# Optimization experiments

Measured on AMD Instinct MI355X. Metric: run time of the kernel, lower is better.

Reference implementation:

```python
import jax, jax.numpy as jnp
import numpy as np

B = 512      # batch of scenes
K = 16       # entities (slots) per scene
H = 500      # h == HIDDEN_SIZE (required by fc2 input width 2*HIDDEN_SIZE)
A = 64       # action_size
EPS = 1e-5


def layernorm(x, g, b):
    mu = jnp.mean(x, axis=-1, keepdims=True)
    var = jnp.var(x, axis=-1, keepdims=True)
    return (x - mu) * jax.lax.rsqrt(var + EPS) * g + b


def setup_inputs() -> dict:
    key = jax.random.key(0)
    ks = jax.random.split(key, 40)
    def W(i, shape, scale=0.02):
        return (jax.random.normal(ks[i], shape, dtype=jnp.float32) * scale)
    inp = {
        "state": jax.random.normal(ks[0], (B * K, H), dtype=jnp.float32),
        "actions": jax.random.normal(ks[1], (B, A), dtype=jnp.float32),
        # action path
        "ac_fc1_w": W(2, (A, H)), "ac_fc1_b": jnp.zeros((H,), jnp.float32),
        "ac_ln1_g": jnp.ones((H,), jnp.float32), "ac_ln1_b": jnp.zeros((H,), jnp.float32),
        "ac_fc2_w": W(3, (2 * H, H)), "ac_fc2_b": jnp.zeros((H,), jnp.float32),
        "ac_lnf2_w": W(4, (H, H)), "ac_lnf2_b": jnp.zeros((H,), jnp.float32),  # ac_ln_f2 is a Linear in the source
        "ac_fc3_w": W(5, (2 * H, 1)), "ac_fc3_b": jnp.zeros((1,), jnp.float32),
        # main path
        "fc1_w": W(6, (H, H)), "fc1_b": jnp.zeros((H,), jnp.float32),
        "ln1_g": jnp.ones((H,), jnp.float32), "ln1_b": jnp.zeros((H,), jnp.float32),
        "fc2_w": W(7, (2 * H, H)), "fc2_b": jnp.zeros((H,), jnp.float32),
        "ln2_g": jnp.ones((H,), jnp.float32), "ln2_b": jnp.zeros((H,), jnp.float32),
        "fc3_w": W(8, (H, H)), "fc3_b": jnp.zeros((H,), jnp.float32),
        "ln3_g": jnp.ones((H,), jnp.float32), "ln3_b": jnp.zeros((H,), jnp.float32),
        "fc4_w": W(9, (H, 100)), "fc4_b": jnp.zeros((100,), jnp.float32),
        "ln4_g": jnp.ones((100,), jnp.float32), "ln4_b": jnp.zeros((100,), jnp.float32),
        "fc5_w": W(10, (100, 1)), "fc5_b": jnp.zeros((1,), jnp.float32),
        "fc6_w": W(11, (2 * H, H)), "fc6_b": jnp.zeros((H,), jnp.float32),
        "ln6_g": jnp.ones((H,), jnp.float32), "ln6_b": jnp.zeros((H,), jnp.float32),
    }
    return inp


def reference(state, actions,
              ac_fc1_w, ac_fc1_b, ac_ln1_g, ac_ln1_b,
              ac_fc2_w, ac_fc2_b, ac_lnf2_w, ac_lnf2_b, ac_fc3_w, ac_fc3_b,
              fc1_w, fc1_b, ln1_g, ln1_b,
              fc2_w, fc2_b, ln2_g, ln2_b,
              fc3_w, fc3_b, ln3_g, ln3_b,
              fc4_w, fc4_b, ln4_g, ln4_b,
              fc5_w, fc5_b,
              fc6_w, fc6_b, ln6_g, ln6_b):
    b, k, h, nc = B, K, H, K - 1

    # ---- action_forward (has_action=True) ----
    a = layernorm(actions @ ac_fc1_w + ac_fc1_b, ac_ln1_g, ac_ln1_b)      # [b, h]
    a = jnp.broadcast_to(a[:, None, :], (b, k, h)).reshape(b * k, h)       # repeat over k
    concat_a = jnp.concatenate([state, a], axis=1)                          # [b*k, 2h]
    attention_a = jax.nn.sigmoid(concat_a @ ac_fc3_w + ac_fc3_b)           # [b*k, 1]
    effect = (concat_a @ ac_fc2_w + ac_fc2_b) @ ac_lnf2_w + ac_lnf2_b      # ac_ln_f2 is Linear
    state = effect * attention_a                                            # [b*k, h]

    # ---- per-entity encoder ----
    s1 = jax.nn.relu(layernorm(state @ fc1_w + fc1_b, ln1_g, ln1_b))       # [b*k, h]
    s1r = s1.reshape(b, k, h)

    # ---- all-pairs context gather: for each i, all j != i ----
    idx = np.array([[j for j in range(k) if j != i] for i in range(k)])    # [k, k-1] static
    cs = s1r[:, idx, :]                                                     # [b, k, k-1, h]
    fs = jnp.broadcast_to(s1r[:, :, None, :], (b, k, nc, h))               # [b, k, k-1, h]
    pair = jnp.concatenate([fs, cs], axis=-1).reshape(b * k * nc, 2 * h)   # [b*k*(k-1), 2h]

    # ---- edge MLP ----
    core = jax.nn.relu(layernorm(pair @ fc2_w + fc2_b, ln2_g, ln2_b))      # [b*k*nc, h]
    context = jax.nn.relu(layernorm(core @ fc3_w + fc3_b, ln3_g, ln3_b))
    context = context.reshape(b * k, nc, h)

    # ---- attention-weighted sum aggregation ----
    att = jnp.tanh(layernorm(core @ fc4_w + fc4_b, ln4_g, ln4_b))          # [b*k*nc, 100]
    att = jax.nn.sigmoid(att @ fc5_w + fc5_b).reshape(b * k, nc, 1)
    effect_sum = jnp.sum(context * att, axis=1)                             # [b*k, h]

    # ---- update ----
    total = jnp.concatenate([s1, effect_sum], axis=1)                       # [b*k, 2h]
    h_new = layernorm(total @ fc6_w + fc6_b, ln6_g, ln6_b)                  # [b*k, h]
    return h_new
```

## Files before the change

kernel.cpp:

```cpp
#include <hip/hip_runtime.h>
#include <math.h>


#define EPSF 1e-5f
typedef unsigned short u16;
typedef unsigned int u32;

typedef __bf16 bf16x8 __attribute__((ext_vector_type(8)));
typedef float f32x4 __attribute__((ext_vector_type(4)));
typedef u16 u16x8 __attribute__((ext_vector_type(8)));

__device__ __forceinline__ float bf2f(u16 u) {
  return __builtin_bit_cast(float, (u32)u << 16);
}
__device__ __forceinline__ u16 f2bf(float f) {
  u32 u = __builtin_bit_cast(u32, f);
  return (u16)((u + 0x7FFFu + ((u >> 16) & 1u)) >> 16);
}

#define GLOAD16(g, l) __builtin_amdgcn_global_load_lds( \
    (__attribute__((address_space(1))) u32*)(g), \
    (__attribute__((address_space(3))) u32*)(l), 16, 0, 0)

template <typename TOUT>
__global__ __launch_bounds__(256) void gemm_mfma(
    const u16* __restrict__ A, const u16* __restrict__ A2,
    const u16* __restrict__ Bt,
    const float* __restrict__ bias, const float* __restrict__ rowscale,
    TOUT* __restrict__ C, int M, int Npad, int K, int lda, int khalf)
{
  __shared__ __align__(16) u16 As[2][128 * 64];
  __shared__ __align__(16) u16 Bs[2][64 * 64];
  const int tid = threadIdx.x;
  const int lane = tid & 63, wid = tid >> 6;

  const int ncols = gridDim.x;
  const int nwg = ncols * gridDim.y;
  const int bid = blockIdx.y * ncols + blockIdx.x;
  const int swz = (bid & 7) * (nwg >> 3) + (bid >> 3);
  const size_t row0 = (size_t)(swz / ncols) * 128;
  const size_t col0 = (size_t)(swz % ncols) * 64;

  f32x4 acc[2][4] = {};

  const int s_sub = tid >> 3;
  const int s_chunk = (tid & 7) ^ (s_sub & 7);
  const size_t aoff = (row0 + s_sub) * (size_t)lda + s_chunk * 8;
  const u16* gA = A + aoff;
  const u16* gA2 = A2 ? (A2 + aoff - khalf) : nullptr;
  const u16* gB = Bt + (col0 + s_sub) * (size_t)K + s_chunk * 8;

  const int fr = lane & 15, fq = lane >> 4;
  const int cx0 = fq ^ (fr & 7);
  const int cx1 = (4 + fq) ^ (fr & 7);

  const int nkt = K >> 6;
  int cur = 0;

  {
#pragma unroll
    for (int h = 0; h < 4; ++h)
      GLOAD16(gA + (size_t)h * 32 * lda, &As[0][(h * 256 + tid) * 8]);
#pragma unroll
    for (int h = 0; h < 2; ++h)
      GLOAD16(gB + (size_t)h * 32 * K, &Bs[0][(h * 256 + tid) * 8]);
  }

  for (int kt = 0; kt < nkt; ++kt) {
    if (kt + 1 < nkt) {
      const int kk = (kt + 1) * 64;
      const u16* a = (A2 && kk >= khalf) ? (gA2 + kk) : (gA + kk);
      const u16* b = gB + kk;
#pragma unroll
      for (int h = 0; h < 4; ++h)
        GLOAD16(a + (size_t)h * 32 * lda, &As[cur ^ 1][(h * 256 + tid) * 8]);
#pragma unroll
      for (int h = 0; h < 2; ++h)
        GLOAD16(b + (size_t)h * 32 * K, &Bs[cur ^ 1][(h * 256 + tid) * 8]);
      asm volatile("s_waitcnt vmcnt(6)" ::: "memory");
    } else {
      asm volatile("s_waitcnt vmcnt(0)" ::: "memory");
    }
    __builtin_amdgcn_sched_barrier(0);
    __builtin_amdgcn_s_barrier();
    __builtin_amdgcn_sched_barrier(0);

    const u16* as = As[cur];
    const u16* bs = Bs[cur];
#pragma unroll
    for (int ks = 0; ks < 2; ++ks) {
      const int cx = ks ? cx1 : cx0;
      bf16x8 af[2], bf[4];
#pragma unroll
      for (int m = 0; m < 2; ++m) {
        int row = wid * 32 + m * 16 + fr;
        af[m] = *reinterpret_cast<const bf16x8*>(as + (row * 8 + cx) * 8);
      }
#pragma unroll
      for (int n = 0; n < 4; ++n) {
        int row = n * 16 + fr;
        bf[n] = *reinterpret_cast<const bf16x8*>(bs + (row * 8 + cx) * 8);
      }
#pragma unroll
      for (int m = 0; m < 2; ++m)
#pragma unroll
        for (int n = 0; n < 4; ++n)
          acc[m][n] = __builtin_amdgcn_mfma_f32_16x16x32_bf16(af[m], bf[n], acc[m][n], 0, 0, 0);
    }
    asm volatile("s_waitcnt lgkmcnt(0)" ::: "memory");
    __builtin_amdgcn_sched_barrier(0);
    __builtin_amdgcn_s_barrier();
    __builtin_amdgcn_sched_barrier(0);
    cur ^= 1;
  }

  const int cl = lane & 15, rg = lane >> 4;
#pragma unroll
  for (int m = 0; m < 2; ++m) {
#pragma unroll
    for (int n = 0; n < 4; ++n) {
      size_t col = col0 + n * 16 + cl;
      float bv = bias[col];
#pragma unroll
      for (int r = 0; r < 4; ++r) {
        size_t row = row0 + wid * 32 + m * 16 + rg * 4 + r;
        float v = acc[m][n][r] + bv;
        if (rowscale) v *= rowscale[row];
        if constexpr (sizeof(TOUT) == 2) C[row * Npad + col] = f2bf(v);
        else                             C[row * Npad + col] = v;
      }
    }
  }
}

template <typename TOUT>
__global__ __launch_bounds__(256) void gemm_sq(
    const u16* __restrict__ A, const u16* __restrict__ Bt,
    const float* __restrict__ bias,
    TOUT* __restrict__ C, int M, int Npad, int K, int lda)
{
  __shared__ __align__(16) u16 As[128 * 64];
  __shared__ __align__(16) u16 Bs[128 * 64];
  const int tid = threadIdx.x;
  const int lane = tid & 63, wid = tid >> 6;
  const int ar0 = (wid >> 1) * 64;
  const int bc0 = (wid & 1) * 64;

  const int ncols = gridDim.x;
  const int nwg = ncols * gridDim.y;
  const int bid = blockIdx.y * ncols + blockIdx.x;
  const int swz = (bid & 7) * (nwg >> 3) + (bid >> 3);
  const size_t row0 = (size_t)(swz / ncols) * 128;
  const size_t col0 = (size_t)(swz % ncols) * 128;

  f32x4 acc[4][4] = {};

  const int s_sub = tid >> 3;
  const int s_chunk = (tid & 7) ^ (s_sub & 7);
  const u16* gA = A + (row0 + s_sub) * (size_t)lda + s_chunk * 8;
  const u16* gB = Bt + (col0 + s_sub) * (size_t)K + s_chunk * 8;

  const int fr = lane & 15, fq = lane >> 4;
  const int cx0 = fq ^ (fr & 7);
  const int cx1 = (4 + fq) ^ (fr & 7);

  for (int kk = 0; kk < K; kk += 64) {
#pragma unroll
    for (int h = 0; h < 4; ++h) {
      GLOAD16(gA + kk + (size_t)h * 32 * lda, &As[(h * 256 + tid) * 8]);
      GLOAD16(gB + kk + (size_t)h * 32 * K,  &Bs[(h * 256 + tid) * 8]);
    }
    __syncthreads();
#pragma unroll
    for (int ks = 0; ks < 2; ++ks) {
      const int cx = ks ? cx1 : cx0;
      bf16x8 af[4], bf[4];
#pragma unroll
      for (int m = 0; m < 4; ++m)
        af[m] = *reinterpret_cast<const bf16x8*>(As + ((ar0 + m * 16 + fr) * 8 + cx) * 8);
#pragma unroll
      for (int n = 0; n < 4; ++n)
        bf[n] = *reinterpret_cast<const bf16x8*>(Bs + ((bc0 + n * 16 + fr) * 8 + cx) * 8);
#pragma unroll
      for (int m = 0; m < 4; ++m)
#pragma unroll
        for (int n = 0; n < 4; ++n)
          acc[m][n] = __builtin_amdgcn_mfma_f32_16x16x32_bf16(af[m], bf[n], acc[m][n], 0, 0, 0);
    }
    __syncthreads();
  }

  const int cl = lane & 15, rg = lane >> 4;
#pragma unroll
  for (int m = 0; m < 4; ++m) {
#pragma unroll
    for (int n = 0; n < 4; ++n) {
      size_t col = col0 + bc0 + n * 16 + cl;
      float bv = bias[col];
#pragma unroll
      for (int r = 0; r < 4; ++r) {
        size_t row = row0 + ar0 + m * 16 + rg * 4 + r;
        float v = acc[m][n][r] + bv;
        if constexpr (sizeof(TOUT) == 2) C[row * Npad + col] = f2bf(v);
        else                             C[row * Npad + col] = v;
      }
    }
  }
}

__global__ __launch_bounds__(256) void gemm128(
    const float* __restrict__ A, const float* __restrict__ B,
    const float* __restrict__ bias, float* __restrict__ C, int M, int N, int K)
{
  __shared__ float As[16][132];
  __shared__ float Bs[16][128];
  const int tid = threadIdx.x;
  const int tx = tid & 15, ty = tid >> 4;
  const int row0 = blockIdx.y * 128, col0 = blockIdx.x * 128;
  float acc[8][8];
#pragma unroll
  for (int i = 0; i < 8; ++i)
#pragma unroll
    for (int j = 0; j < 8; ++j) acc[i][j] = 0.f;

  const int nkt = (K + 15) >> 4;
  for (int kt = 0; kt < nkt; ++kt) {
    const int k0 = kt << 4;
#pragma unroll
    for (int h = 0; h < 2; ++h) {
      int i = tid + h * 256;
      int m = i >> 2, kk = (i & 3) << 2;
      int gm = row0 + m, gk = k0 + kk;
      float4 v = make_float4(0.f, 0.f, 0.f, 0.f);
      if (gm < M && gk < K) v = *reinterpret_cast<const float4*>(A + (size_t)gm * K + gk);
      As[kk + 0][m] = v.x; As[kk + 1][m] = v.y; As[kk + 2][m] = v.z; As[kk + 3][m] = v.w;
    }
#pragma unroll
    for (int h = 0; h < 2; ++h) {
      int i = tid + h * 256;
      int kk = i >> 5, n = (i & 31) << 2;
      int gk = k0 + kk, gn = col0 + n;
      float4 v = make_float4(0.f, 0.f, 0.f, 0.f);
      if (gk < K && gn < N) v = *reinterpret_cast<const float4*>(B + (size_t)gk * N + gn);
      *reinterpret_cast<float4*>(&Bs[kk][n]) = v;
    }
    __syncthreads();
#pragma unroll
    for (int kk = 0; kk < 16; ++kk) {
      float4 a0 = *reinterpret_cast<const float4*>(&As[kk][ty * 4]);
      float4 a1 = *reinterpret_cast<const float4*>(&As[kk][ty * 4 + 64]);
      float4 b0 = *reinterpret_cast<const float4*>(&Bs[kk][tx * 4]);
      float4 b1 = *reinterpret_cast<const float4*>(&Bs[kk][tx * 4 + 64]);
      float av[8] = {a0.x, a0.y, a0.z, a0.w, a1.x, a1.y, a1.z, a1.w};
      float bv[8] = {b0.x, b0.y, b0.z, b0.w, b1.x, b1.y, b1.z, b1.w};
#pragma unroll
      for (int i = 0; i < 8; ++i)
#pragma unroll
        for (int j = 0; j < 8; ++j) acc[i][j] += av[i] * bv[j];
    }
    __syncthreads();
  }
#pragma unroll
  for (int i = 0; i < 8; ++i) {
    int gm = row0 + ty * 4 + ((i >> 2) << 6) + (i & 3);
    if (gm >= M) continue;
#pragma unroll
    for (int j = 0; j < 8; ++j) {
      int gn = col0 + tx * 4 + ((j >> 2) << 6) + (j & 3);
      if (gn < N) C[(size_t)gm * N + gn] = acc[i][j] + bias[gn];
    }
  }
}

template <int ACT, typename TIN, typename TOUT>
__global__ __launch_bounds__(256) void ln_wave4(
    const TIN* __restrict__ X, TOUT* __restrict__ Y,
    const float* __restrict__ g, const float* __restrict__ b,
    int ldx, int ldy)
{
  int w = threadIdx.x >> 6, lane = threadIdx.x & 63;
  int id0 = (blockIdx.x * 4 + w) * 4;
  int k0 = lane * 8;
  float xv[4][8], s[4], s2[4];
#pragma unroll
  for (int r = 0; r < 4; ++r) {
    s[r] = 0.f; s2[r] = 0.f;
    if constexpr (sizeof(TIN) == 2) {
      u16x8 u = *reinterpret_cast<const u16x8*>((const u16*)X + (size_t)(id0 + r) * ldx + k0);
#pragma unroll
      for (int e = 0; e < 8; ++e) xv[r][e] = bf2f(u[e]);
    } else {
      const float* x = (const float*)X + (size_t)(id0 + r) * ldx;
      if (k0 + 8 <= 500) {
        float4 a = *reinterpret_cast<const float4*>(x + k0);
        float4 c = *reinterpret_cast<const float4*>(x + k0 + 4);
        xv[r][0] = a.x; xv[r][1] = a.y; xv[r][2] = a.z; xv[r][3] = a.w;
        xv[r][4] = c.x; xv[r][5] = c.y; xv[r][6] = c.z; xv[r][7] = c.w;
      } else {
#pragma unroll
        for (int e = 0; e < 8; ++e) xv[r][e] = (k0 + e < 500) ? x[k0 + e] : 0.f;
      }
    }
#pragma unroll
    for (int e = 0; e < 8; ++e) { s[r] += xv[r][e]; s2[r] += xv[r][e] * xv[r][e]; }
  }
#pragma unroll
  for (int m = 32; m; m >>= 1)
#pragma unroll
    for (int r = 0; r < 4; ++r) {
      s[r] += __shfl_xor(s[r], m);
      s2[r] += __shfl_xor(s2[r], m);
    }
  float gv[8], bv[8];
#pragma unroll
  for (int e = 0; e < 8; ++e) {
    int k = k0 + e;
    gv[e] = (k < 500) ? g[k] : 0.f;
    bv[e] = (k < 500) ? b[k] : 0.f;
  }
#pragma unroll
  for (int r = 0; r < 4; ++r) {
    float mu = s[r] / 500.f;
    float rstd = rsqrtf(s2[r] / 500.f - mu * mu + EPSF);
    float ov[8];
#pragma unroll
    for (int e = 0; e < 8; ++e) {
      float v = (k0 + e < 500) ? ((xv[r][e] - mu) * rstd * gv[e] + bv[e]) : 0.f;
      if (ACT == 1) v = fmaxf(v, 0.f);
      ov[e] = v;
    }
    if constexpr (sizeof(TOUT) == 2) {
      u16x8 o;
#pragma unroll
      for (int e = 0; e < 8; ++e) o[e] = f2bf(ov[e]);
      *reinterpret_cast<u16x8*>((u16*)Y + (size_t)(id0 + r) * ldy + k0) = o;
    } else {
      float* y = (float*)Y + (size_t)(id0 + r) * ldy;
      if (k0 + 4 <= 500)
        *reinterpret_cast<float4*>(y + k0) = make_float4(ov[0], ov[1], ov[2], ov[3]);
      if (k0 + 8 <= 500)
        *reinterpret_cast<float4*>(y + k0 + 4) = make_float4(ov[4], ov[5], ov[6], ov[7]);
    }
  }
}

__global__ __launch_bounds__(256) void build_concat(
    const float* __restrict__ state, const u16* __restrict__ a, u16* __restrict__ cat)
{
  int r = blockIdx.x, t = threadIdx.x;
  int b = r >> 4;
  u16* c = cat + (size_t)r * 1024;
  if (t < 125) {
    float4 v = *reinterpret_cast<const float4*>(state + (size_t)r * 500 + t * 4);
    ushort4 o; o.x = f2bf(v.x); o.y = f2bf(v.y); o.z = f2bf(v.z); o.w = f2bf(v.w);
    *reinterpret_cast<ushort4*>(c + t * 4) = o;
    *reinterpret_cast<ushort4*>(c + 500 + t * 4) =
        *reinterpret_cast<const ushort4*>(a + (size_t)b * 512 + t * 4);
  }
  if (t < 24) c[1000 + t] = 0;
}

__global__ __launch_bounds__(256) void dot_sig4(
    const u16* __restrict__ cat, const float* __restrict__ w3,
    const float* __restrict__ b3, float* __restrict__ atta)
{
  int w = threadIdx.x >> 6, lane = threadIdx.x & 63;
  int r0 = (blockIdx.x * 4 + w) * 4;
  int k0 = lane * 16;
  float wv[16];
#pragma unroll
  for (int e = 0; e < 16; ++e) wv[e] = (k0 + e < 1000) ? w3[k0 + e] : 0.f;
  float s[4];
#pragma unroll
  for (int r = 0; r < 4; ++r) {
    const u16* x = cat + (size_t)(r0 + r) * 1024 + k0;
    u16x8 u0 = *reinterpret_cast<const u16x8*>(x);
    u16x8 u1 = *reinterpret_cast<const u16x8*>(x + 8);
    float acc = 0.f;
#pragma unroll
    for (int e = 0; e < 8; ++e) acc += bf2f(u0[e]) * wv[e];
#pragma unroll
    for (int e = 0; e < 8; ++e) acc += bf2f(u1[e]) * wv[8 + e];
    s[r] = acc;
  }
#pragma unroll
  for (int m = 32; m; m >>= 1)
#pragma unroll
    for (int r = 0; r < 4; ++r) s[r] += __shfl_xor(s[r], m);
  if (lane == 0) {
#pragma unroll
    for (int r = 0; r < 4; ++r)
      atta[r0 + r] = 1.f / (1.f + expf(-(s[r] + b3[0])));
  }
}

__global__ __launch_bounds__(256) void core_build3(
    const u16* __restrict__ PQ, u16* __restrict__ core,
    const float* __restrict__ g2, const float* __restrict__ b2, int c0)
{
  int w = threadIdx.x >> 6, lane = threadIdx.x & 63;
  int id0 = (blockIdx.x * 4 + w) * 4;
  int k0 = lane * 8;
  u16x8 up[4], uq[4];
#pragma unroll
  for (int r = 0; r < 4; ++r) {
    int id = id0 + r;
    int pp = id / 15, j = id - pp * 15;
    int gp = c0 + pp, i = gp & 15;
    int col = j + (j >= i);
    int r2 = (gp & ~15) | col;
    up[r] = *reinterpret_cast<const u16x8*>(PQ + (size_t)gp * 1024 + k0);
    uq[r] = *reinterpret_cast<const u16x8*>(PQ + (size_t)r2 * 1024 + 512 + k0);
  }
  float xv[4][8], s[4], s2[4];
#pragma unroll
  for (int r = 0; r < 4; ++r) {
    s[r] = 0.f; s2[r] = 0.f;
#pragma unroll
    for (int e = 0; e < 8; ++e) {
      float v = bf2f(up[r][e]) + bf2f(uq[r][e]);
      xv[r][e] = v; s[r] += v; s2[r] += v * v;
    }
  }
#pragma unroll
  for (int m = 32; m; m >>= 1)
#pragma unroll
    for (int r = 0; r < 4; ++r) {
      s[r] += __shfl_xor(s[r], m);
      s2[r] += __shfl_xor(s2[r], m);
    }
  float gv[8], bv[8];
#pragma unroll
  for (int e = 0; e < 8; ++e) {
    int k = k0 + e;
    gv[e] = (k < 500) ? g2[k] : 0.f;
    bv[e] = (k < 500) ? b2[k] : 0.f;
  }
#pragma unroll
  for (int r = 0; r < 4; ++r) {
    float mu = s[r] / 500.f;
    float rstd = rsqrtf(s2[r] / 500.f - mu * mu + EPSF);
    u16x8 o;
#pragma unroll
    for (int e = 0; e < 8; ++e)
      o[e] = (k0 + e < 500) ? f2bf(fmaxf((xv[r][e] - mu) * rstd * gv[e] + bv[e], 0.f)) : (u16)0;
    *reinterpret_cast<u16x8*>(core + (size_t)(id0 + r) * 512 + k0) = o;
  }
}

__global__ __launch_bounds__(256) void chunk_post3(
    const u16* __restrict__ V,
    const float* __restrict__ g3, const float* __restrict__ b3,
    const float* __restrict__ g4, const float* __restrict__ b4,
    const float* __restrict__ w5, const float* __restrict__ b5,
    u16* __restrict__ esum16, int c0)
{
  __shared__ u16 rows[15][512];
  __shared__ float st[15][4];
  int pp = blockIdx.x, t = threadIdx.x;
  int lane = t & 63, w = t >> 6;
  int k0 = lane * 8;
  int kk = lane * 2;

  u16x8 u[4]; ushort2 ua[4];
#pragma unroll
  for (int r = 0; r < 4; ++r) {
    int j = w * 4 + r;
    if (j < 15) {
      const u16* vr = V + (size_t)(pp * 15 + j) * 640;
      u[r] = *reinterpret_cast<const u16x8*>(vr + k0);
      ua[r] = *reinterpret_cast<const ushort2*>(vr + 512 + kk);
    }
  }
  float s[4], s2[4], sa[4], sa2[4], y0[4], y1[4];
#pragma unroll
  for (int r = 0; r < 4; ++r) {
    s[r] = s2[r] = sa[r] = sa2[r] = 0.f; y0[r] = y1[r] = 0.f;
    int j = w * 4 + r;
    if (j < 15) {
#pragma unroll
      for (int e = 0; e < 8; ++e) { float v = bf2f(u[r][e]); s[r] += v; s2[r] += v * v; }
      y0[r] = bf2f(ua[r].x); y1[r] = bf2f(ua[r].y);
      sa[r] = y0[r] + y1[r]; sa2[r] = y0[r] * y0[r] + y1[r] * y1[r];
      *reinterpret_cast<u16x8*>(&rows[j][k0]) = u[r];
    }
  }
#pragma unroll
  for (int m = 32; m; m >>= 1)
#pragma unroll
    for (int r = 0; r < 4; ++r) {
      s[r]   += __shfl_xor(s[r], m);
      s2[r]  += __shfl_xor(s2[r], m);
      sa[r]  += __shfl_xor(sa[r], m);
      sa2[r] += __shfl_xor(sa2[r], m);
    }
  float dv[4];
#pragma unroll
  for (int r = 0; r < 4; ++r) {
    float mu4 = sa[r] / 100.f;
    float rstd4 = rsqrtf(sa2[r] / 100.f - mu4 * mu4 + EPSF);
    float d = 0.f;
    if (kk < 100)     d += tanhf((y0[r] - mu4) * rstd4 * g4[kk] + b4[kk]) * w5[kk];
    if (kk + 1 < 100) d += tanhf((y1[r] - mu4) * rstd4 * g4[kk + 1] + b4[kk + 1]) * w5[kk + 1];
    dv[r] = d;
  }
#pragma unroll
  for (int m = 32; m; m >>= 1)
#pragma unroll
    for (int r = 0; r < 4; ++r) dv[r] += __shfl_xor(dv[r], m);
  if (lane == 0) {
#pragma unroll
    for (int r = 0; r < 4; ++r) {
      int j = w * 4 + r;
      if (j < 15) {
        float mu = s[r] / 500.f;
        st[j][0] = mu;
        st[j][1] = rsqrtf(s2[r] / 500.f - mu * mu + EPSF);
        st[j][2] = 1.f / (1.f + expf(-(dv[r] + b5[0])));
      }
    }
  }
  __syncthreads();

  u16* o = esum16 + (size_t)(c0 + pp) * 512;
  for (int n = t; n < 500; n += 256) {
    float gg = g3[n], bb = b3[n], acc = 0.f;
#pragma unroll
    for (int j = 0; j < 15; ++j) {
      float v = bf2f(rows[j][n]);
      acc += fmaxf((v - st[j][0]) * st[j][1] * gg + bb, 0.f) * st[j][2];
    }
    o[n] = f2bf(acc);
  }
  if (t < 12) o[500 + t] = 0;
}

struct TJob {
  const float* src; u16* dst;
  int K, N, srcLd, ldDst, nOff, kOff, tileBase, tilesX;
};
struct TJobs { TJob j[9]; int total; };

__global__ void pack_weights(TJobs jobs)
{
  __shared__ float tl[32][33];
  int bid = blockIdx.x;
  int ji = 0;
#pragma unroll
  for (int q = 1; q < 9; ++q) if (bid >= jobs.j[q].tileBase) ji = q;
  const TJob& J = jobs.j[ji];
  int t = bid - J.tileBase;
  int bx = t % J.tilesX, by = t / J.tilesX;
  int tx = threadIdx.x, ty = threadIdx.y;
  int k0 = by * 32, n0 = bx * 32;
#pragma unroll
  for (int r = 0; r < 4; ++r) {
    int row = k0 + ty + r * 8;
    if (row < J.K && n0 + tx < J.N) tl[ty + r * 8][tx] = J.src[(size_t)row * J.srcLd + n0 + tx];
  }
  __syncthreads();
#pragma unroll
  for (int r = 0; r < 4; ++r) {
    int n = n0 + ty + r * 8, k = k0 + tx;
    if (n < J.N && k < J.K)
      J.dst[(size_t)(n + J.nOff) * J.ldDst + J.kOff + k] = f2bf(tl[tx][ty + r * 8]);
  }
}

__global__ void pack_biases(
    const float* ac2, const float* lnf2, const float* f1, const float* f2,
    const float* f3, const float* f4, const float* f6,
    float* b_ac2p, float* b_lnf2p, float* b_f1p, float* b2p, float* b34p, float* b_f6p)
{
  int t = threadIdx.x;
  switch (blockIdx.x) {
    case 0: if (t < 512) b_ac2p[t]  = (t < 500) ? ac2[t]  : 0.f; break;
    case 1: if (t < 512) b_lnf2p[t] = (t < 500) ? lnf2[t] : 0.f; break;
    case 2: if (t < 512) b_f1p[t]   = (t < 500) ? f1[t]   : 0.f; break;
    case 3: b2p[t] = (t < 500) ? f2[t] : 0.f; break;
    case 4: if (t < 640) b34p[t] = (t < 500) ? f3[t] : ((t >= 512 && t < 612) ? f4[t - 512] : 0.f); break;
    case 5: if (t < 512) b_f6p[t]   = (t < 500) ? f6[t]   : 0.f; break;
  }
}

extern "C" void kernel_launch(void* const* d_in, const int* in_sizes, int n_in,
                              void* d_out, int out_size, void* d_ws, size_t ws_size,
                              hipStream_t stream)
{
  const float* state    = (const float*)d_in[0];
  const float* actions  = (const float*)d_in[1];
  const float* ac_fc1_w = (const float*)d_in[2];
  const float* ac_fc1_b = (const float*)d_in[3];
  const float* ac_ln1_g = (const float*)d_in[4];
  const float* ac_ln1_b = (const float*)d_in[5];
  const float* ac_fc2_w = (const float*)d_in[6];
  const float* ac_fc2_b = (const float*)d_in[7];
  const float* ac_lnf2_w= (const float*)d_in[8];
  const float* ac_lnf2_b= (const float*)d_in[9];
  const float* ac_fc3_w = (const float*)d_in[10];
  const float* ac_fc3_b = (const float*)d_in[11];
  const float* fc1_w = (const float*)d_in[12];
  const float* fc1_b = (const float*)d_in[13];
  const float* ln1_g = (const float*)d_in[14];
  const float* ln1_b = (const float*)d_in[15];
  const float* fc2_w = (const float*)d_in[16];
  const float* fc2_b = (const float*)d_in[17];
  const float* ln2_g = (const float*)d_in[18];
  const float* ln2_b = (const float*)d_in[19];
  const float* fc3_w = (const float*)d_in[20];
  const float* fc3_b = (const float*)d_in[21];
  const float* ln3_g = (const float*)d_in[22];
  const float* ln3_b = (const float*)d_in[23];
  const float* fc4_w = (const float*)d_in[24];
  const float* fc4_b = (const float*)d_in[25];
  const float* ln4_g = (const float*)d_in[26];
  const float* ln4_b = (const float*)d_in[27];
  const float* fc5_w = (const float*)d_in[28];
  const float* fc5_b = (const float*)d_in[29];
  const float* fc6_w = (const float*)d_in[30];
  const float* fc6_b = (const float*)d_in[31];
  const float* ln6_g = (const float*)d_in[32];
  const float* ln6_b = (const float*)d_in[33];
  float* out = (float*)d_out;

  char* p = (char*)d_ws;
  auto carve = [&](size_t bytes) { char* r = p; p += (bytes + 255) & ~(size_t)255; return r; };
  u16*   cat    = (u16*)  carve(8192ull * 1024 * 2);
  u16*   t1     = (u16*)  carve(8192ull * 512 * 2);
  u16*   s2     = (u16*)  carve(8192ull * 512 * 2);
  u16*   s1     = (u16*)  carve(8192ull * 512 * 2);
  u16*   core   = (u16*)  carve(61440ull * 512 * 2);
  u16*   v      = (u16*)  carve(61440ull * 640 * 2);
  u16*   PQ     = (u16*)  carve(8192ull * 1024 * 2);
  u16*   esum16 = (u16*)  carve(8192ull * 512 * 2);
  u16*   a_buf  = (u16*)  carve(512ull * 512 * 2);
  float* tmp_a  = (float*)carve(512ull * 500 * 4);
  float* att_a  = (float*)carve(8192ull * 4);
  char*  wT0    =         carve(0);
  u16*   ac_fc2T  = (u16*)carve(512ull * 1024 * 2);
  u16*   ac_lnf2T = (u16*)carve(512ull * 512 * 2);
  u16*   fc1T     = (u16*)carve(512ull * 512 * 2);
  u16*   B2T      = (u16*)carve(1024ull * 512 * 2);
  u16*   B34T     = (u16*)carve(640ull * 512 * 2);
  u16*   fc6T     = (u16*)carve(512ull * 1024 * 2);
  size_t wTbytes  = (size_t)((char*)carve(0) - wT0);
  float* b_ac2p  = (float*)carve(512 * 4);
  float* b_lnf2p = (float*)carve(512 * 4);
  float* b_f1p   = (float*)carve(512 * 4);
  float* b2p     = (float*)carve(1024 * 4);
  float* b34p    = (float*)carve(640 * 4);
  float* b_f6p   = (float*)carve(512 * 4);

  dim3 blk(256);
  dim3 tblk(32, 8);

  hipMemsetAsync(wT0, 0, wTbytes, stream);
  TJobs jobs;
  int base = 0;
  auto addjob = [&](int idx, const float* src, u16* dst, int K, int N, int srcLd,
                    int ldDst, int nOff, int kOff) {
    int tx = (N + 31) / 32, ty = (K + 31) / 32;
    jobs.j[idx] = {src, dst, K, N, srcLd, ldDst, nOff, kOff, base, tx};
    base += tx * ty;
  };
  addjob(0, ac_fc2_w,         ac_fc2T,  1000, 500, 500, 1024, 0, 0);
  addjob(1, ac_lnf2_w,        ac_lnf2T,  500, 500, 500,  512, 0, 0);
  addjob(2, fc1_w,            fc1T,      500, 500, 500,  512, 0, 0);
  addjob(3, fc2_w,            B2T,       500, 500, 500,  512, 0, 0);
  addjob(4, fc2_w + 250000,   B2T,       500, 500, 500,  512, 512, 0);
  addjob(5, fc3_w,            B34T,      500, 500, 500,  512, 0, 0);
  addjob(6, fc4_w,            B34T,      500, 100, 100,  512, 512, 0);
  addjob(7, fc6_w,            fc6T,      500, 500, 500, 1024, 0, 0);
  addjob(8, fc6_w + 250000,   fc6T,      500, 500, 500, 1024, 0, 512);
  jobs.total = base;
  pack_weights<<<base, tblk, 0, stream>>>(jobs);
  pack_biases<<<6, 1024, 0, stream>>>(ac_fc2_b, ac_lnf2_b, fc1_b, fc2_b, fc3_b, fc4_b, fc6_b,
                                      b_ac2p, b_lnf2p, b_f1p, b2p, b34p, b_f6p);

  gemm128<<<dim3(4, 4), blk, 0, stream>>>(actions, ac_fc1_w, ac_fc1_b, tmp_a, 512, 500, 64);
  ln_wave4<0, float, u16><<<32, blk, 0, stream>>>(tmp_a, a_buf, ac_ln1_g, ac_ln1_b, 500, 512);
  build_concat<<<8192, blk, 0, stream>>>(state, a_buf, cat);

  gemm_mfma<u16><<<dim3(8, 64), blk, 0, stream>>>(cat, nullptr, ac_fc2T, b_ac2p, nullptr,
                                                  t1, 8192, 512, 1024, 1024, 0);
  dot_sig4<<<512, blk, 0, stream>>>(cat, ac_fc3_w, ac_fc3_b, att_a);
  gemm_mfma<u16><<<dim3(8, 64), blk, 0, stream>>>(t1, nullptr, ac_lnf2T, b_lnf2p, att_a,
                                                  s2, 8192, 512, 512, 512, 0);
  gemm_mfma<u16><<<dim3(8, 64), blk, 0, stream>>>(s2, nullptr, fc1T, b_f1p, nullptr,
                                                  t1, 8192, 512, 512, 512, 0);
  ln_wave4<1, u16, u16><<<512, blk, 0, stream>>>(t1, s1, ln1_g, ln1_b, 512, 512);
  gemm_mfma<u16><<<dim3(16, 64), blk, 0, stream>>>(s1, nullptr, B2T, b2p, nullptr,
                                                   PQ, 8192, 1024, 512, 512, 0);

  for (int c = 0; c < 2; ++c) {
    int c0 = c * 4096;
    core_build3<<<3840, blk, 0, stream>>>(PQ, core, ln2_g, ln2_b, c0);
    gemm_sq<u16><<<dim3(5, 480), blk, 0, stream>>>(core, B34T, b34p,
                                                   v, 61440, 640, 512, 512);
    chunk_post3<<<4096, blk, 0, stream>>>(v, ln3_g, ln3_b, ln4_g, ln4_b, fc5_w, fc5_b,
                                          esum16, c0);
  }

  gemm_mfma<u16><<<dim3(8, 64), blk, 0, stream>>>(s1, esum16, fc6T, b_f6p, nullptr,
                                                  t1, 8192, 512, 1024, 512, 512);
  ln_wave4<0, u16, float><<<512, blk, 0, stream>>>(t1, out, ln6_g, ln6_b, 512, 500);
}
```

Before: 427.5 us.

## Fold three chained linear layers into one precomputed weight product

The three consecutive GEMMs (ac_fc2, ac_lnf2 with row scaling by the attention scalar, then fc1) have no nonlinearity between them. They are collapsed into one 8192x1024x512 GEMM against a precomputed product W_ac2·W_lnf2·W_fc1. The folded bias is applied as rowscale*(b_ac2·W_lnf2·W_fc1 + b_lnf2·W_fc1) + b_fc1. Small per-call GEMMs and matvecs build the fused weight and bias, removing two large GEMMs and an intermediate buffer. The cost is extra bf16 rounding in the precomputed product and a few extra small launches.

```diff
diff --git a/kernel.cpp b/kernel.cpp
--- a/kernel.cpp
+++ b/kernel.cpp
@@ -22,12 +22,13 @@
     (__attribute__((address_space(1))) u32*)(g), \
     (__attribute__((address_space(3))) u32*)(l), 16, 0, 0)
 
-template <typename TOUT>
+template <typename TOUT, bool TRANSC = false>
 __global__ __launch_bounds__(256) void gemm_mfma(
     const u16* __restrict__ A, const u16* __restrict__ A2,
     const u16* __restrict__ Bt,
     const float* __restrict__ bias, const float* __restrict__ rowscale,
-    TOUT* __restrict__ C, int M, int Npad, int K, int lda, int khalf)
+    const float* __restrict__ bias2,
+    TOUT* __restrict__ C, int M, int Npad, int K, int lda, int khalf, int ldc)
 {
   __shared__ __align__(16) u16 As[2][128 * 64];
   __shared__ __align__(16) u16 Bs[2][64 * 64];
@@ -121,13 +122,24 @@
     for (int n = 0; n < 4; ++n) {
       size_t col = col0 + n * 16 + cl;
       float bv = bias[col];
-#pragma unroll
-      for (int r = 0; r < 4; ++r) {
-        size_t row = row0 + wid * 32 + m * 16 + rg * 4 + r;
-        float v = acc[m][n][r] + bv;
-        if (rowscale) v *= rowscale[row];
-        if constexpr (sizeof(TOUT) == 2) C[row * Npad + col] = f2bf(v);
-        else                             C[row * Npad + col] = v;
+      if constexpr (TRANSC) {
+        size_t row0m = row0 + wid * 32 + m * 16 + rg * 4;
+        ushort4 o;
+        o.x = f2bf(acc[m][n][0] + bv);
+        o.y = f2bf(acc[m][n][1] + bv);
+        o.z = f2bf(acc[m][n][2] + bv);
+        o.w = f2bf(acc[m][n][3] + bv);
+        *reinterpret_cast<ushort4*>((u16*)C + col * (size_t)ldc + row0m) = o;
+      } else {
+#pragma unroll
+        for (int r = 0; r < 4; ++r) {
+          size_t row = row0 + wid * 32 + m * 16 + rg * 4 + r;
+          float v = acc[m][n][r] + bv;
+          if (rowscale) v *= rowscale[row];
+          if (bias2) v += bias2[col];
+          if constexpr (sizeof(TOUT) == 2) C[row * (size_t)ldc + col] = f2bf(v);
+          else                             C[row * (size_t)ldc + col] = v;
+        }
       }
     }
   }
@@ -394,6 +406,20 @@
   }
 }
 
+__global__ __launch_bounds__(256) void matvec_col(
+    const float* __restrict__ x, const float* __restrict__ W,
+    const float* __restrict__ add, float* __restrict__ y, int J, int N, int ld)
+{
+  int n = blockIdx.x * 256 + threadIdx.x;
+  if (n >= 512) return;
+  float acc = 0.f;
+  if (n < N) {
+    for (int j = 0; j < J; ++j) acc += x[j] * W[(size_t)j * ld + n];
+    if (add) acc += add[n];
+  }
+  y[n] = acc;
+}
+
 __global__ __launch_bounds__(256) void core_build3(
     const u16* __restrict__ PQ, u16* __restrict__ core,
     const float* __restrict__ g2, const float* __restrict__ b2, int c0)
@@ -537,7 +563,7 @@
 
 struct TJob {
   const float* src; u16* dst;
-  int K, N, srcLd, ldDst, nOff, kOff, tileBase, tilesX;
+  int K, N, srcLd, ldDst, nOff, kOff, tileBase, tilesX, trans;
 };
 struct TJobs { TJob j[9]; int total; };
 
@@ -553,33 +579,41 @@
   int bx = t % J.tilesX, by = t / J.tilesX;
   int tx = threadIdx.x, ty = threadIdx.y;
   int k0 = by * 32, n0 = bx * 32;
-#pragma unroll
-  for (int r = 0; r < 4; ++r) {
-    int row = k0 + ty + r * 8;
-    if (row < J.K && n0 + tx < J.N) tl[ty + r * 8][tx] = J.src[(size_t)row * J.srcLd + n0 + tx];
-  }
-  __syncthreads();
-#pragma unroll
-  for (int r = 0; r < 4; ++r) {
-    int n = n0 + ty + r * 8, k = k0 + tx;
-    if (n < J.N && k < J.K)
-      J.dst[(size_t)(n + J.nOff) * J.ldDst + J.kOff + k] = f2bf(tl[tx][ty + r * 8]);
+  if (J.trans) {
+#pragma unroll
+    for (int r = 0; r < 4; ++r) {
+      int row = k0 + ty + r * 8;
+      if (row < J.K && n0 + tx < J.N) tl[ty + r * 8][tx] = J.src[(size_t)row * J.srcLd + n0 + tx];
+    }
+    __syncthreads();
+#pragma unroll
+    for (int r = 0; r < 4; ++r) {
+      int n = n0 + ty + r * 8, k = k0 + tx;
+      if (n < J.N && k < J.K)
+        J.dst[(size_t)(n + J.nOff) * J.ldDst + J.kOff + k] = f2bf(tl[tx][ty + r * 8]);
+    }
+  } else {
+#pragma unroll
+    for (int r = 0; r < 4; ++r) {
+      int row = k0 + ty + r * 8, n = n0 + tx;
+      if (row < J.K && n < J.N)
+        J.dst[(size_t)(row + J.kOff) * J.ldDst + J.nOff + n] =
+            f2bf(J.src[(size_t)row * J.srcLd + n]);
+    }
   }
 }
 
 __global__ void pack_biases(
-    const float* ac2, const float* lnf2, const float* f1, const float* f2,
-    const float* f3, const float* f4, const float* f6,
-    float* b_ac2p, float* b_lnf2p, float* b_f1p, float* b2p, float* b34p, float* b_f6p)
+    const float* f1, const float* f2, const float* f3, const float* f4,
+    const float* f6,
+    float* b_f1p, float* b2p, float* b34p, float* b_f6p)
 {
   int t = threadIdx.x;
   switch (blockIdx.x) {
-    case 0: if (t < 512) b_ac2p[t]  = (t < 500) ? ac2[t]  : 0.f; break;
-    case 1: if (t < 512) b_lnf2p[t] = (t < 500) ? lnf2[t] : 0.f; break;
-    case 2: if (t < 512) b_f1p[t]   = (t < 500) ? f1[t]   : 0.f; break;
-    case 3: b2p[t] = (t < 500) ? f2[t] : 0.f; break;
-    case 4: if (t < 640) b34p[t] = (t < 500) ? f3[t] : ((t >= 512 && t < 612) ? f4[t - 512] : 0.f); break;
-    case 5: if (t < 512) b_f6p[t]   = (t < 500) ? f6[t]   : 0.f; break;
+    case 0: if (t < 512) b_f1p[t] = (t < 500) ? f1[t] : 0.f; break;
+    case 1: b2p[t] = (t < 500) ? f2[t] : 0.f; break;
+    case 2: if (t < 640) b34p[t] = (t < 500) ? f3[t] : ((t >= 512 && t < 612) ? f4[t - 512] : 0.f); break;
+    case 3: if (t < 512) b_f6p[t] = (t < 500) ? f6[t] : 0.f; break;
   }
 }
 
@@ -627,7 +661,6 @@
   auto carve = [&](size_t bytes) { char* r = p; p += (bytes + 255) & ~(size_t)255; return r; };
   u16*   cat    = (u16*)  carve(8192ull * 1024 * 2);
   u16*   t1     = (u16*)  carve(8192ull * 512 * 2);
-  u16*   s2     = (u16*)  carve(8192ull * 512 * 2);
   u16*   s1     = (u16*)  carve(8192ull * 512 * 2);
   u16*   core   = (u16*)  carve(61440ull * 512 * 2);
   u16*   v      = (u16*)  carve(61440ull * 640 * 2);
@@ -637,19 +670,22 @@
   float* tmp_a  = (float*)carve(512ull * 500 * 4);
   float* att_a  = (float*)carve(8192ull * 4);
   char*  wT0    =         carve(0);
-  u16*   ac_fc2T  = (u16*)carve(512ull * 1024 * 2);
+  u16*   ac_fc2P  = (u16*)carve(1024ull * 512 * 2);
   u16*   ac_lnf2T = (u16*)carve(512ull * 512 * 2);
   u16*   fc1T     = (u16*)carve(512ull * 512 * 2);
   u16*   B2T      = (u16*)carve(1024ull * 512 * 2);
   u16*   B34T     = (u16*)carve(640ull * 512 * 2);
   u16*   fc6T     = (u16*)carve(512ull * 1024 * 2);
+  u16*   W12      = (u16*)carve(1024ull * 512 * 2);
+  u16*   W3T      = (u16*)carve(512ull * 1024 * 2);
+  float* z512     = (float*)carve(512 * 4);
   size_t wTbytes  = (size_t)((char*)carve(0) - wT0);
-  float* b_ac2p  = (float*)carve(512 * 4);
-  float* b_lnf2p = (float*)carve(512 * 4);
   float* b_f1p   = (float*)carve(512 * 4);
   float* b2p     = (float*)carve(1024 * 4);
   float* b34p    = (float*)carve(640 * 4);
   float* b_f6p   = (float*)carve(512 * 4);
+  float* t512    = (float*)carve(512 * 4);
+  float* c3      = (float*)carve(512 * 4);
 
   dim3 blk(256);
   dim3 tblk(32, 8);
@@ -658,39 +694,44 @@
   TJobs jobs;
   int base = 0;
   auto addjob = [&](int idx, const float* src, u16* dst, int K, int N, int srcLd,
-                    int ldDst, int nOff, int kOff) {
+                    int ldDst, int nOff, int kOff, int trans) {
     int tx = (N + 31) / 32, ty = (K + 31) / 32;
-    jobs.j[idx] = {src, dst, K, N, srcLd, ldDst, nOff, kOff, base, tx};
+    jobs.j[idx] = {src, dst, K, N, srcLd, ldDst, nOff, kOff, base, tx, trans};
     base += tx * ty;
   };
-  addjob(0, ac_fc2_w,         ac_fc2T,  1000, 500, 500, 1024, 0, 0);
-  addjob(1, ac_lnf2_w,        ac_lnf2T,  500, 500, 500,  512, 0, 0);
-  addjob(2, fc1_w,            fc1T,      500, 500, 500,  512, 0, 0);
-  addjob(3, fc2_w,            B2T,       500, 500, 500,  512, 0, 0);
-  addjob(4, fc2_w + 250000,   B2T,       500, 500, 500,  512, 512, 0);
-  addjob(5, fc3_w,            B34T,      500, 500, 500,  512, 0, 0);
-  addjob(6, fc4_w,            B34T,      500, 100, 100,  512, 512, 0);
-  addjob(7, fc6_w,            fc6T,      500, 500, 500, 1024, 0, 0);
-  addjob(8, fc6_w + 250000,   fc6T,      500, 500, 500, 1024, 0, 512);
+  addjob(0, ac_fc2_w,       ac_fc2P, 1000, 500, 500,  512, 0, 0, 0);
+  addjob(1, ac_lnf2_w,      ac_lnf2T, 500, 500, 500,  512, 0, 0, 1);
+  addjob(2, fc1_w,          fc1T,     500, 500, 500,  512, 0, 0, 1);
+  addjob(3, fc2_w,          B2T,      500, 500, 500,  512, 0, 0, 1);
+  addjob(4, fc2_w + 250000, B2T,      500, 500, 500,  512, 512, 0, 1);
+  addjob(5, fc3_w,          B34T,     500, 500, 500,  512, 0, 0, 1);
+  addjob(6, fc4_w,          B34T,     500, 100, 100,  512, 512, 0, 1);
+  addjob(7, fc6_w,          fc6T,     500, 500, 500, 1024, 0, 0, 1);
+  addjob(8, fc6_w + 250000, fc6T,     500, 500, 500, 1024, 0, 512, 1);
   jobs.total = base;
   pack_weights<<<base, tblk, 0, stream>>>(jobs);
-  pack_biases<<<6, 1024, 0, stream>>>(ac_fc2_b, ac_lnf2_b, fc1_b, fc2_b, fc3_b, fc4_b, fc6_b,
-                                      b_ac2p, b_lnf2p, b_f1p, b2p, b34p, b_f6p);
+  pack_biases<<<4, 1024, 0, stream>>>(fc1_b, fc2_b, fc3_b, fc4_b, fc6_b,
+                                      b_f1p, b2p, b34p, b_f6p);
+
+  gemm_mfma<u16><<<dim3(8, 8), blk, 0, stream>>>(ac_fc2P, nullptr, ac_lnf2T, z512,
+                                                 nullptr, nullptr, W12,
+                                                 1024, 512, 512, 512, 0, 512);
+  gemm_mfma<u16, true><<<dim3(8, 8), blk, 0, stream>>>(W12, nullptr, fc1T, z512,
+                                                       nullptr, nullptr, W3T,
+                                                       1024, 512, 512, 512, 0, 1024);
+  matvec_col<<<2, blk, 0, stream>>>(ac_fc2_b, ac_lnf2_w, ac_lnf2_b, t512, 500, 500, 500);
+  matvec_col<<<2, blk, 0, stream>>>(t512, fc1_w, nullptr, c3, 500, 500, 500);
 
   gemm128<<<dim3(4, 4), blk, 0, stream>>>(actions, ac_fc1_w, ac_fc1_b, tmp_a, 512, 500, 64);
   ln_wave4<0, float, u16><<<32, blk, 0, stream>>>(tmp_a, a_buf, ac_ln1_g, ac_ln1_b, 500, 512);
   build_concat<<<8192, blk, 0, stream>>>(state, a_buf, cat);
-
-  gemm_mfma<u16><<<dim3(8, 64), blk, 0, stream>>>(cat, nullptr, ac_fc2T, b_ac2p, nullptr,
-                                                  t1, 8192, 512, 1024, 1024, 0);
   dot_sig4<<<512, blk, 0, stream>>>(cat, ac_fc3_w, ac_fc3_b, att_a);
-  gemm_mfma<u16><<<dim3(8, 64), blk, 0, stream>>>(t1, nullptr, ac_lnf2T, b_lnf2p, att_a,
-                                                  s2, 8192, 512, 512, 512, 0);
-  gemm_mfma<u16><<<dim3(8, 64), blk, 0, stream>>>(s2, nullptr, fc1T, b_f1p, nullptr,
-                                                  t1, 8192, 512, 512, 512, 0);
+
+  gemm_mfma<u16><<<dim3(8, 64), blk, 0, stream>>>(cat, nullptr, W3T, c3, att_a, b_f1p,
+                                                  t1, 8192, 512, 1024, 1024, 0, 512);
   ln_wave4<1, u16, u16><<<512, blk, 0, stream>>>(t1, s1, ln1_g, ln1_b, 512, 512);
-  gemm_mfma<u16><<<dim3(16, 64), blk, 0, stream>>>(s1, nullptr, B2T, b2p, nullptr,
-                                                   PQ, 8192, 1024, 512, 512, 0);
+  gemm_mfma<u16><<<dim3(16, 64), blk, 0, stream>>>(s1, nullptr, B2T, b2p, nullptr, nullptr,
+                                                   PQ, 8192, 1024, 512, 512, 0, 1024);
 
   for (int c = 0; c < 2; ++c) {
     int c0 = c * 4096;
@@ -701,7 +742,7 @@
                                           esum16, c0);
   }
 
-  gemm_mfma<u16><<<dim3(8, 64), blk, 0, stream>>>(s1, esum16, fc6T, b_f6p, nullptr,
-                                                  t1, 8192, 512, 1024, 512, 512);
+  gemm_mfma<u16><<<dim3(8, 64), blk, 0, stream>>>(s1, esum16, fc6T, b_f6p, nullptr, nullptr,
+                                                  t1, 8192, 512, 1024, 512, 512, 512);
   ln_wave4<0, u16, float><<<512, blk, 0, stream>>>(t1, out, ln6_g, ln6_b, 512, 500);
 }
```

Result: slower. 664.8 us (+55.5%).
